# Kernel optimization log

Hardware: AMD Instinct MI355X
Metric: run time of the kernel (lower is better)

Reference implementation:

```python
import jax, jax.numpy as jnp
import numpy as np

B, S, D, H, DK, DV = 2, 2048, 1024, 16, 64, 64


def setup_inputs() -> dict:
    key = jax.random.key(0)
    ks = jax.random.split(key, 12)
    inp = {
        "query": jax.random.normal(ks[0], (B, S, D), jnp.float32),
        "key":   jax.random.normal(ks[1], (B, S, D), jnp.float32),
        "value": jax.random.normal(ks[2], (B, S, D), jnp.float32),
        # additive mask broadcast over per-head [B,S,S] scores (zeros = no masking)
        "mask":  jnp.zeros((S, S), jnp.float32),
        # stacked per-head projection params (math-equivalent to H separate Linears)
        "Wq": jax.random.normal(ks[3], (H, D, DK), jnp.float32) / np.sqrt(D),
        "bq": jax.random.normal(ks[4], (H, DK), jnp.float32) * 0.02,
        "Wk": jax.random.normal(ks[5], (H, D, DK), jnp.float32) / np.sqrt(D),
        "bk": jax.random.normal(ks[6], (H, DK), jnp.float32) * 0.02,
        "Wv": jax.random.normal(ks[7], (H, D, DV), jnp.float32) / np.sqrt(D),
        "bv": jax.random.normal(ks[8], (H, DV), jnp.float32) * 0.02,
        "Wo": jax.random.normal(ks[9], (H * DV, D), jnp.float32) / np.sqrt(H * DV),
        "bo": jax.random.normal(ks[10], (D,), jnp.float32) * 0.02,
    }
    return inp


def reference(query, key, value, mask, Wq, bq, Wk, bk, Wv, bv, Wo, bo):
    # per-head projections, vectorized over heads
    q = jnp.einsum("bsd,hdk->bhsk", query, Wq) + bq[None, :, None, :]
    k = jnp.einsum("bsd,hdk->bhsk", key, Wk) + bk[None, :, None, :]
    v = jnp.einsum("bsd,hdv->bhsv", value, Wv) + bv[None, :, None, :]
    # explicit QK^T softmax V, scale by sqrt(dim_k) (key.size(-1))
    scores = jnp.einsum("bhsk,bhtk->bhst", q, k) / jnp.sqrt(jnp.asarray(DK, q.dtype))
    scores = scores + mask  # broadcast [S,S] -> [B,H,S,S]
    attn = jax.nn.softmax(scores, axis=-1)
    out = jnp.einsum("bhst,bhtv->bhsv", attn, v)
    # concat heads along last dim: [B,S,H*DV]
    out = out.transpose(0, 2, 1, 3).reshape(B, S, H * DV)
    return out @ Wo + bo
```

## Files before the change

kernel.cpp:

```cpp
#include <hip/hip_runtime.h>
#include <stdint.h>

typedef __bf16 bf16;
typedef float f32x4 __attribute__((ext_vector_type(4)));
typedef __bf16 bf16x8 __attribute__((ext_vector_type(8)));
typedef __bf16 bf16x4 __attribute__((ext_vector_type(4)));

__device__ __forceinline__ void async_load16(const void* g, void* l) {
    __builtin_amdgcn_global_load_lds(
        (const __attribute__((address_space(1))) void*)g,
        (__attribute__((address_space(3))) void*)l, 16, 0, 0);
}

__global__ void detect_dtype(const unsigned short* __restrict__ q, int* __restrict__ flag) {
    __shared__ int cnt;
    if (threadIdx.x == 0) cnt = 0;
    __syncthreads();
    int c = 0;
    for (int i = threadIdx.x; i < 4096; i += 256) {
        int e = (q[i] >> 7) & 0xFF;
        if (e >= 0xC0) ++c;
    }
    atomicAdd(&cnt, c);
    __syncthreads();
    if (threadIdx.x == 0) { flag[0] = (cnt > 64) ? 1 : 0; flag[1] = 0; }
}

__global__ void maskscan(const unsigned int* __restrict__ m,
                         const int* __restrict__ flag, int* __restrict__ nz) {
    const int f = flag[0];
    const long nvec = (f ? 4194304L : 2097152L) / 4;
    unsigned int acc = 0;
    long stride = (long)gridDim.x * blockDim.x;
    for (long i = (long)blockIdx.x * blockDim.x + threadIdx.x; i < nvec; i += stride) {
        uint4 v = ((const uint4*)m)[i];
        acc |= v.x | v.y | v.z | v.w;
    }
    if (acc) atomicOr(nz, 1);
}

__global__ void convert2(const void* __restrict__ x0, const void* __restrict__ x1,
                         bf16* __restrict__ o0, bf16* __restrict__ o1,
                         const int* __restrict__ flag) {
    const int f = *flag;
    const void* x = blockIdx.z ? x1 : x0;
    bf16* o = blockIdx.z ? o1 : o0;
    size_t i = ((size_t)blockIdx.x * 256 + threadIdx.x) * 8;
    if (f) {
        f32x4 a = ((const f32x4*)x)[i / 4];
        f32x4 b = ((const f32x4*)x)[i / 4 + 1];
        bf16x8 v;
        for (int j = 0; j < 4; ++j) { v[j] = (bf16)a[j]; v[4 + j] = (bf16)b[j]; }
        *(bf16x8*)(o + i) = v;
    } else {
        *(bf16x8*)(o + i) = *(const bf16x8*)((const bf16*)x + i);
    }
}

__global__ void transpose_w3(const void* __restrict__ w0, const void* __restrict__ w1,
                             const void* __restrict__ w2, bf16* __restrict__ out,
                             const int* __restrict__ flag) {
    __shared__ bf16 t[32][33];
    const int f = *flag;
    const int z = blockIdx.z, src = z >> 4, sub = z & 15;
    const void* in = (src == 0) ? w0 : ((src == 1) ? w1 : w2);
    size_t base = (size_t)sub * 65536;
    int c0 = blockIdx.x * 32, r0 = blockIdx.y * 32;
    int tx = threadIdx.x, ty = threadIdx.y;
    if (f) {
        const float* inF = (const float*)in;
        for (int i = 0; i < 32; i += 8)
            t[ty + i][tx] = (bf16)inF[base + (size_t)(r0 + ty + i) * 64 + (c0 + tx)];
    } else {
        const bf16* inB = (const bf16*)in;
        for (int i = 0; i < 32; i += 8)
            t[ty + i][tx] = inB[base + (size_t)(r0 + ty + i) * 64 + (c0 + tx)];
    }
    __syncthreads();
    bf16* o = out + (size_t)z * 65536;
    for (int i = 0; i < 32; i += 8)
        o[(size_t)(c0 + ty + i) * 1024 + (r0 + tx)] = t[tx][ty + i];
}

__global__ void transpose_wo(const void* __restrict__ in, bf16* __restrict__ out,
                             const int* __restrict__ flag) {
    __shared__ bf16 t[32][33];
    const int f = *flag;
    int c0 = blockIdx.x * 32, r0 = blockIdx.y * 32;
    int tx = threadIdx.x, ty = threadIdx.y;
    if (f) {
        const float* inF = (const float*)in;
        for (int i = 0; i < 32; i += 8)
            t[ty + i][tx] = (bf16)inF[(size_t)(r0 + ty + i) * 1024 + (c0 + tx)];
    } else {
        const bf16* inB = (const bf16*)in;
        for (int i = 0; i < 32; i += 8)
            t[ty + i][tx] = inB[(size_t)(r0 + ty + i) * 1024 + (c0 + tx)];
    }
    __syncthreads();
    for (int i = 0; i < 32; i += 8)
        out[(size_t)(c0 + ty + i) * 1024 + (r0 + tx)] = t[tx][ty + i];
}

__global__ __launch_bounds__(256, 3) void gemm_qkv_b(
    const bf16* __restrict__ A0, const bf16* __restrict__ A1,
    const bf16* __restrict__ Bt,
    const void* __restrict__ b0, const void* __restrict__ b1, const void* __restrict__ b2,
    bf16* __restrict__ Qp, bf16* __restrict__ Kp, bf16* __restrict__ Vt,
    const int* __restrict__ flag, int zbase) {
    __shared__ __attribute__((aligned(16))) bf16 As[128 * 64];
    __shared__ __attribute__((aligned(16))) bf16 Bs[128 * 64];

    const int f = flag[0];
    const int K = 1024, N = 1024;
    const int z = zbase + blockIdx.z;
    const bf16* A    = blockIdx.z ? A1 : A0;
    const void* bias = (z == 0) ? b0 : ((z == 1) ? b1 : b2);
    const bf16* B    = Bt + (size_t)z * 1024 * 1024;

    const int tid  = threadIdx.x;
    const int lane = tid & 63;
    const int w    = tid >> 6;
    const int quad = lane >> 4;
    const int mrow = lane & 15;
    const int m0 = blockIdx.y * 128;
    const int n0 = blockIdx.x * 128;
    const int wm = (w & 1) * 64;
    const int wn = (w >> 1) * 64;

    f32x4 acc[4][4] = {};

    for (int k0 = 0; k0 < K; k0 += 64) {
        for (int it = 0; it < 4; ++it) {
            int ci  = it * 256 + tid;
            int row = ci >> 3, pc = ci & 7;
            int gc  = pc ^ (row & 7);
            async_load16(A + (size_t)(m0 + row) * K + k0 + gc * 8,
                         As + (size_t)(it * 256 + w * 64) * 8);
            async_load16(B + (size_t)(n0 + row) * K + k0 + gc * 8,
                         Bs + (size_t)(it * 256 + w * 64) * 8);
        }
        __syncthreads();
        for (int kk = 0; kk < 2; ++kk) {
            bf16x8 afr[4], bfr[4];
            for (int mi = 0; mi < 4; ++mi) {
                int row = wm + mi * 16 + mrow;
                int pc  = (kk * 4 + quad) ^ (row & 7);
                afr[mi] = *(const bf16x8*)(As + row * 64 + pc * 8);
            }
            for (int ni = 0; ni < 4; ++ni) {
                int row = wn + ni * 16 + mrow;
                int pc  = (kk * 4 + quad) ^ (row & 7);
                bfr[ni] = *(const bf16x8*)(Bs + row * 64 + pc * 8);
            }
            for (int mi = 0; mi < 4; ++mi)
                for (int ni = 0; ni < 4; ++ni)
                    acc[mi][ni] = __builtin_amdgcn_mfma_f32_16x16x32_bf16(
                        afr[mi], bfr[ni], acc[mi][ni], 0, 0, 0);
        }
        __syncthreads();
    }

    const float scl = (z == 0) ? 0.18033688f : 1.0f;
    for (int ni = 0; ni < 4; ++ni) {
        int n    = n0 + wn + ni * 16 + mrow;
        float bv = f ? ((const float*)bias)[n] : (float)((const bf16*)bias)[n];
        for (int mi = 0; mi < 4; ++mi) {
            int mb = m0 + wm + mi * 16 + quad * 4;
            if (z == 2) {
                bf16x4 pk;
                for (int r = 0; r < 4; ++r) pk[r] = (bf16)(acc[mi][ni][r] + bv);
                *(bf16x4*)(Vt + (((size_t)(mb >> 11) * 1024 + n) << 11) + (mb & 2047)) = pk;
            } else {
                bf16* P = (z == 0) ? Qp : Kp;
                for (int r = 0; r < 4; ++r)
                    P[(size_t)(mb + r) * N + n] = (bf16)((acc[mi][ni][r] + bv) * scl);
            }
        }
    }
}

__global__ __launch_bounds__(256, 2) void gemm_out(
    const bf16* __restrict__ A, const bf16* __restrict__ Bt,
    const void* __restrict__ bias, void* __restrict__ Cout,
    const int* __restrict__ flag) {
    __shared__ __attribute__((aligned(16))) bf16 As[128 * 64];
    __shared__ __attribute__((aligned(16))) bf16 Bs[64 * 64];

    const int f = flag[0];
    const int K = 1024, N = 1024;
    const int tid  = threadIdx.x;
    const int lane = tid & 63;
    const int w    = tid >> 6;
    const int quad = lane >> 4;
    const int mrow = lane & 15;
    const int m0 = blockIdx.y * 128;
    const int n0 = blockIdx.x * 64;
    const int wm = (w & 1) * 64;
    const int wn = (w >> 1) * 32;

    f32x4 acc[4][2] = {};

    for (int k0 = 0; k0 < K; k0 += 64) {
        for (int it = 0; it < 4; ++it) {
            int ci  = it * 256 + tid;
            int row = ci >> 3, pc = ci & 7;
            int gc  = pc ^ (row & 7);
            async_load16(A + (size_t)(m0 + row) * K + k0 + gc * 8,
                         As + (size_t)(it * 256 + w * 64) * 8);
        }
        for (int it = 0; it < 2; ++it) {
            int ci  = it * 256 + tid;
            int row = ci >> 3, pc = ci & 7;
            int gc  = pc ^ (row & 7);
            async_load16(Bt + (size_t)(n0 + row) * K + k0 + gc * 8,
                         Bs + (size_t)(it * 256 + w * 64) * 8);
        }
        __syncthreads();
        for (int kk = 0; kk < 2; ++kk) {
            bf16x8 afr[4], bfr[2];
            for (int mi = 0; mi < 4; ++mi) {
                int row = wm + mi * 16 + mrow;
                int pc  = (kk * 4 + quad) ^ (row & 7);
                afr[mi] = *(const bf16x8*)(As + row * 64 + pc * 8);
            }
            for (int ni = 0; ni < 2; ++ni) {
                int row = wn + ni * 16 + mrow;
                int pc  = (kk * 4 + quad) ^ (row & 7);
                bfr[ni] = *(const bf16x8*)(Bs + row * 64 + pc * 8);
            }
            for (int mi = 0; mi < 4; ++mi)
                for (int ni = 0; ni < 2; ++ni)
                    acc[mi][ni] = __builtin_amdgcn_mfma_f32_16x16x32_bf16(
                        afr[mi], bfr[ni], acc[mi][ni], 0, 0, 0);
        }
        __syncthreads();
    }

    for (int ni = 0; ni < 2; ++ni) {
        int n    = n0 + wn + ni * 16 + mrow;
        float bv = f ? ((const float*)bias)[n] : (float)((const bf16*)bias)[n];
        for (int mi = 0; mi < 4; ++mi) {
            int mb = m0 + wm + mi * 16 + quad * 4;
            for (int r = 0; r < 4; ++r) {
                float val = acc[mi][ni][r] + bv;
                if (f) ((float*)Cout)[(size_t)(mb + r) * N + n] = val;
                else   ((bf16*)Cout)[(size_t)(mb + r) * N + n] = (bf16)val;
            }
        }
    }
}

__global__ __launch_bounds__(256, 3) void flash_attn(
    const bf16* __restrict__ Qp, const bf16* __restrict__ Kp,
    const bf16* __restrict__ Vt, const void* __restrict__ maskv,
    bf16* __restrict__ O, const int* __restrict__ flag) {
    __shared__ __attribute__((aligned(16))) bf16 Ks[2][4096];
    __shared__ __attribute__((aligned(16))) bf16 Vs[2][4096];
    __shared__ __attribute__((aligned(16))) bf16 Ps[64 * 72];

    const int f       = flag[0];
    const int useMask = flag[1];
    const int tid  = threadIdx.x;
    const int lane = tid & 63;
    const int w    = tid >> 6;
    const int quad = lane >> 4;
    const int c    = lane & 15;
    const int s0   = blockIdx.x * 64;
    const int h    = blockIdx.y;
    const int b    = blockIdx.z;

    const size_t qkBase = (size_t)b * 2048 * 1024 + h * 64;
    const size_t vtBase = ((size_t)b * 1024 + h * 64) * 2048;

    const int ci0 = tid, ci1 = 256 + tid;
    const int r0 = ci0 >> 3, g0 = (ci0 & 7) ^ (r0 & 7);
    const int r1 = ci1 >> 3, g1 = (ci1 & 7) ^ (r1 & 7);
    const bf16* kp0 = Kp + qkBase + (size_t)r0 * 1024 + g0 * 8;
    const bf16* kp1 = Kp + qkBase + (size_t)r1 * 1024 + g1 * 8;
    const bf16* vp0 = Vt + vtBase + (size_t)r0 * 2048 + g0 * 8;
    const bf16* vp1 = Vt + vtBase + (size_t)r1 * 2048 + g1 * 8;

#define STAGE(B_, T_) do {                                              \
        async_load16(kp0 + (size_t)(T_) * 1024, &Ks[B_][(size_t)(w * 64) * 8]);        \
        async_load16(kp1 + (size_t)(T_) * 1024, &Ks[B_][(size_t)(256 + w * 64) * 8]);  \
        async_load16(vp0 + (T_),                &Vs[B_][(size_t)(w * 64) * 8]);        \
        async_load16(vp1 + (T_),                &Vs[B_][(size_t)(256 + w * 64) * 8]);  \
    } while (0)

    const bf16* kf0 = &Ks[0][c * 64 + ((0 + quad) ^ (c & 7)) * 8];
    const bf16* kf1 = &Ks[0][c * 64 + ((4 + quad) ^ (c & 7)) * 8];
    const bf16* vf0 = &Vs[0][c * 64 + ((0 + quad) ^ (c & 7)) * 8];
    const bf16* vf1 = &Vs[0][c * 64 + ((4 + quad) ^ (c & 7)) * 8];
    bf16*       pw  = Ps + (w * 16 + c) * 72 + quad * 4;
    const bf16* pr  = Ps + (w * 16 + c) * 72 + quad * 8;

    bf16x8 aq[2];
    {
        const bf16* qrow = Qp + qkBase + (size_t)(s0 + w * 16 + c) * 1024;
        aq[0] = *(const bf16x8*)(qrow + quad * 8);
        aq[1] = *(const bf16x8*)(qrow + 32 + quad * 8);
    }

    f32x4 o_acc[4] = {};
    float l_s = 0.f;

    const size_t mbase = (size_t)(s0 + w * 16 + c) * 2048;

#define FCOMP(IB_, T_) do {                                                         \
        f32x4 sc[4] = {};                                                           \
        _Pragma("unroll") for (int tt = 0; tt < 4; ++tt) {                          \
            bf16x8 ak0 = *(const bf16x8*)(kf0 + (IB_) * 4096 + tt * 1024);          \
            bf16x8 ak1 = *(const bf16x8*)(kf1 + (IB_) * 4096 + tt * 1024);          \
            sc[tt] = __builtin_amdgcn_mfma_f32_16x16x32_bf16(ak0, aq[0], sc[tt], 0, 0, 0); \
            sc[tt] = __builtin_amdgcn_mfma_f32_16x16x32_bf16(ak1, aq[1], sc[tt], 0, 0, 0); \
        }                                                                           \
        if (useMask) {                                                              \
            const size_t mr = mbase + (T_);                                         \
            _Pragma("unroll") for (int tt = 0; tt < 4; ++tt) {                      \
                if (f) {                                                            \
                    f32x4 mk = *(const f32x4*)((const float*)maskv + mr + tt * 16 + quad * 4); \
                    for (int r = 0; r < 4; ++r) sc[tt][r] += mk[r] * 1.44269504f;   \
                } else {                                                            \
                    bf16x4 mk = *(const bf16x4*)((const bf16*)maskv + mr + tt * 16 + quad * 4); \
                    for (int r = 0; r < 4; ++r) sc[tt][r] += (float)mk[r] * 1.44269504f; \
                }                                                                   \
            }                                                                       \
        }                                                                           \
        float rsum = 0.f;                                                           \
        _Pragma("unroll") for (int tt = 0; tt < 4; ++tt) {                          \
            bf16x4 pk;                                                              \
            for (int r = 0; r < 4; ++r) {                                           \
                float p = exp2f(sc[tt][r]);                                         \
                rsum += p;                                                          \
                pk[r] = (bf16)p;                                                    \
            }                                                                       \
            *(bf16x4*)(pw + tt * 16) = pk;                                          \
        }                                                                           \
        l_s += rsum;                                                                \
        _Pragma("unroll") for (int kk = 0; kk < 2; ++kk) {                          \
            bf16x8 ap = *(const bf16x8*)(pr + kk * 32);                             \
            const bf16* vfb = kk ? vf1 : vf0;                                       \
            _Pragma("unroll") for (int ni = 0; ni < 4; ++ni) {                      \
                bf16x8 bv = *(const bf16x8*)(vfb + (IB_) * 4096 + ni * 1024);       \
                o_acc[ni] = __builtin_amdgcn_mfma_f32_16x16x32_bf16(ap, bv, o_acc[ni], 0, 0, 0); \
            }                                                                       \
        }                                                                           \
    } while (0)

    STAGE(0, 0);
    for (int t0 = 0; t0 < 2048; t0 += 128) {
        __syncthreads();
        STAGE(1, t0 + 64);
        FCOMP(0, t0);
        __syncthreads();
        if (t0 + 128 < 2048) STAGE(0, t0 + 128);
        FCOMP(1, t0 + 64);
    }
#undef STAGE
#undef FCOMP

    l_s += __shfl_xor(l_s, 16, 64);
    l_s += __shfl_xor(l_s, 32, 64);
    float lrow[4];
    for (int r = 0; r < 4; ++r) lrow[r] = __shfl(l_s, quad * 4 + r, 64);
    for (int r = 0; r < 4; ++r) {
        float inv   = 1.0f / lrow[r];
        size_t roff = (size_t)(b * 2048 + s0 + w * 16 + quad * 4 + r) * 1024 + h * 64;
        for (int ni = 0; ni < 4; ++ni)
            O[roff + ni * 16 + c] = (bf16)(o_acc[ni][r] * inv);
    }
}

extern "C" void kernel_launch(void* const* d_in, const int* in_sizes, int n_in,
                              void* d_out, int out_size, void* d_ws, size_t ws_size,
                              hipStream_t stream) {
    bf16* ws = (bf16*)d_ws;
    (void)in_sizes; (void)n_in; (void)out_size; (void)ws_size;

    const size_t MM = 1024 * 1024;
    int*  flag = (int*)ws;
    bf16* WqT  = ws + 8;
    bf16* WoT  = WqT + 3 * MM;
    bf16* Qp   = WoT + MM;
    bf16* Kp   = Qp + 4 * MM;
    bf16* AO   = Kp + 4 * MM;
    bf16* Xc1  = AO;
    bf16* Vt   = (bf16*)d_out;
    bf16* Xc2  = (bf16*)d_out + 4 * MM;

    detect_dtype<<<1, 256, 0, stream>>>((const unsigned short*)d_in[0], flag);
    maskscan<<<1024, 256, 0, stream>>>((const unsigned int*)d_in[3], flag, flag + 1);

    dim3 tb(32, 8, 1);
    transpose_w3<<<dim3(2, 32, 48), tb, 0, stream>>>(d_in[4], d_in[6], d_in[8], WqT, flag);
    transpose_wo<<<dim3(32, 32, 1), tb, 0, stream>>>(d_in[10], WoT, flag);

    convert2<<<dim3(2048, 1, 2), 256, 0, stream>>>(d_in[0], d_in[1], Xc1, Xc2, flag);
    gemm_qkv_b<<<dim3(8, 32, 2), 256, 0, stream>>>(Xc1, Xc2, WqT,
                                                   d_in[5], d_in[7], d_in[9],
                                                   Qp, Kp, Vt, flag, 0);
    convert2<<<dim3(2048, 1, 1), 256, 0, stream>>>(d_in[2], d_in[2], Xc1, Xc1, flag);
    gemm_qkv_b<<<dim3(8, 32, 1), 256, 0, stream>>>(Xc1, Xc1, WqT,
                                                   d_in[5], d_in[7], d_in[9],
                                                   Qp, Kp, Vt, flag, 2);

    flash_attn<<<dim3(32, 16, 2), 256, 0, stream>>>(Qp, Kp, Vt, d_in[3], AO, flag);

    gemm_out<<<dim3(16, 32, 1), 256, 0, stream>>>(AO, WoT, d_in[11], d_out, flag);
}
```

Before: 303.3 us.

## Fuse prep kernels, single QKV GEMM launch, 128-row flash attention tiles

Merges mask scan, input conversion and all weight transposes into one multi-task prep kernel. The three QKV projections now run in one GEMM launch, with the key input read directly as fp32 and converted to bf16 in LDS instead of via a separate convert pass. Flash attention doubles the query rows per block to 128 so each K/V tile loaded into LDS is reused by twice as many MFMAs, and occupancy is lowered to 2 blocks per CU. This cuts launch count and memory traffic but raises register and LDS pressure in attention and widens the fp32 A tile in the GEMM.

```diff
diff --git a/kernel.cpp b/kernel.cpp
--- a/kernel.cpp
+++ b/kernel.cpp
@@ -26,95 +26,93 @@
     if (threadIdx.x == 0) { flag[0] = (cnt > 64) ? 1 : 0; flag[1] = 0; }
 }
 
-__global__ void maskscan(const unsigned int* __restrict__ m,
-                         const int* __restrict__ flag, int* __restrict__ nz) {
-    const int f = flag[0];
-    const long nvec = (f ? 4194304L : 2097152L) / 4;
-    unsigned int acc = 0;
-    long stride = (long)gridDim.x * blockDim.x;
-    for (long i = (long)blockIdx.x * blockDim.x + threadIdx.x; i < nvec; i += stride) {
-        uint4 v = ((const uint4*)m)[i];
-        acc |= v.x | v.y | v.z | v.w;
-    }
-    if (acc) atomicOr(nz, 1);
-}
-
-__global__ void convert2(const void* __restrict__ x0, const void* __restrict__ x1,
-                         bf16* __restrict__ o0, bf16* __restrict__ o1,
-                         const int* __restrict__ flag) {
-    const int f = *flag;
-    const void* x = blockIdx.z ? x1 : x0;
-    bf16* o = blockIdx.z ? o1 : o0;
-    size_t i = ((size_t)blockIdx.x * 256 + threadIdx.x) * 8;
-    if (f) {
-        f32x4 a = ((const f32x4*)x)[i / 4];
-        f32x4 b = ((const f32x4*)x)[i / 4 + 1];
-        bf16x8 v;
-        for (int j = 0; j < 4; ++j) { v[j] = (bf16)a[j]; v[4 + j] = (bf16)b[j]; }
-        *(bf16x8*)(o + i) = v;
+__global__ void prep(const void* __restrict__ qv, const void* __restrict__ vv,
+                     const void* __restrict__ wq, const void* __restrict__ wk,
+                     const void* __restrict__ wv, const void* __restrict__ wo,
+                     const unsigned int* __restrict__ mask,
+                     bf16* __restrict__ Xq, bf16* __restrict__ Xv,
+                     bf16* __restrict__ WqT, bf16* __restrict__ WoT,
+                     int* __restrict__ flag) {
+    __shared__ bf16 t[32][33];
+    const int f    = flag[0];
+    const int task = blockIdx.z;
+    const int bid  = blockIdx.x + 64 * blockIdx.y;
+
+    if (task < 2) {
+        const void* x = task ? vv : qv;
+        bf16* o = task ? Xv : Xq;
+        size_t i = ((size_t)bid * 256 + threadIdx.x) * 8;
+        if (f) {
+            f32x4 a = ((const f32x4*)x)[i / 4];
+            f32x4 b = ((const f32x4*)x)[i / 4 + 1];
+            bf16x8 v;
+            for (int j = 0; j < 4; ++j) { v[j] = (bf16)a[j]; v[4 + j] = (bf16)b[j]; }
+            *(bf16x8*)(o + i) = v;
+        } else {
+            *(bf16x8*)(o + i) = *(const bf16x8*)((const bf16*)x + i);
+        }
+    } else if (task < 5) {
+        if (bid >= 1024) return;
+        const void* in = (task == 2) ? wq : ((task == 3) ? wk : wv);
+        int sub = bid >> 6, rem = bid & 63;
+        int c0 = (rem & 1) * 32, r0 = (rem >> 1) * 32;
+        int tx = threadIdx.x & 31, ty = threadIdx.x >> 5;
+        size_t base = (size_t)sub * 65536;
+        if (f) {
+            const float* inF = (const float*)in;
+            for (int i = 0; i < 32; i += 8)
+                t[ty + i][tx] = (bf16)inF[base + (size_t)(r0 + ty + i) * 64 + (c0 + tx)];
+        } else {
+            const bf16* inB = (const bf16*)in;
+            for (int i = 0; i < 32; i += 8)
+                t[ty + i][tx] = inB[base + (size_t)(r0 + ty + i) * 64 + (c0 + tx)];
+        }
+        __syncthreads();
+        bf16* o = WqT + ((size_t)(task - 2) * 16 + sub) * 65536;
+        for (int i = 0; i < 32; i += 8)
+            o[(size_t)(c0 + ty + i) * 1024 + (r0 + tx)] = t[tx][ty + i];
+    } else if (task == 5) {
+        if (bid >= 1024) return;
+        int c0 = (bid & 31) * 32, r0 = (bid >> 5) * 32;
+        int tx = threadIdx.x & 31, ty = threadIdx.x >> 5;
+        if (f) {
+            const float* inF = (const float*)wo;
+            for (int i = 0; i < 32; i += 8)
+                t[ty + i][tx] = (bf16)inF[(size_t)(r0 + ty + i) * 1024 + (c0 + tx)];
+        } else {
+            const bf16* inB = (const bf16*)wo;
+            for (int i = 0; i < 32; i += 8)
+                t[ty + i][tx] = inB[(size_t)(r0 + ty + i) * 1024 + (c0 + tx)];
+        }
+        __syncthreads();
+        for (int i = 0; i < 32; i += 8)
+            WoT[(size_t)(c0 + ty + i) * 1024 + (r0 + tx)] = t[tx][ty + i];
     } else {
-        *(bf16x8*)(o + i) = *(const bf16x8*)((const bf16*)x + i);
-    }
-}
-
-__global__ void transpose_w3(const void* __restrict__ w0, const void* __restrict__ w1,
-                             const void* __restrict__ w2, bf16* __restrict__ out,
-                             const int* __restrict__ flag) {
-    __shared__ bf16 t[32][33];
-    const int f = *flag;
-    const int z = blockIdx.z, src = z >> 4, sub = z & 15;
-    const void* in = (src == 0) ? w0 : ((src == 1) ? w1 : w2);
-    size_t base = (size_t)sub * 65536;
-    int c0 = blockIdx.x * 32, r0 = blockIdx.y * 32;
-    int tx = threadIdx.x, ty = threadIdx.y;
-    if (f) {
-        const float* inF = (const float*)in;
-        for (int i = 0; i < 32; i += 8)
-            t[ty + i][tx] = (bf16)inF[base + (size_t)(r0 + ty + i) * 64 + (c0 + tx)];
-    } else {
-        const bf16* inB = (const bf16*)in;
-        for (int i = 0; i < 32; i += 8)
-            t[ty + i][tx] = inB[base + (size_t)(r0 + ty + i) * 64 + (c0 + tx)];
-    }
-    __syncthreads();
-    bf16* o = out + (size_t)z * 65536;
-    for (int i = 0; i < 32; i += 8)
-        o[(size_t)(c0 + ty + i) * 1024 + (r0 + tx)] = t[tx][ty + i];
-}
-
-__global__ void transpose_wo(const void* __restrict__ in, bf16* __restrict__ out,
-                             const int* __restrict__ flag) {
-    __shared__ bf16 t[32][33];
-    const int f = *flag;
-    int c0 = blockIdx.x * 32, r0 = blockIdx.y * 32;
-    int tx = threadIdx.x, ty = threadIdx.y;
-    if (f) {
-        const float* inF = (const float*)in;
-        for (int i = 0; i < 32; i += 8)
-            t[ty + i][tx] = (bf16)inF[(size_t)(r0 + ty + i) * 1024 + (c0 + tx)];
-    } else {
-        const bf16* inB = (const bf16*)in;
-        for (int i = 0; i < 32; i += 8)
-            t[ty + i][tx] = inB[(size_t)(r0 + ty + i) * 1024 + (c0 + tx)];
-    }
-    __syncthreads();
-    for (int i = 0; i < 32; i += 8)
-        out[(size_t)(c0 + ty + i) * 1024 + (r0 + tx)] = t[tx][ty + i];
-}
-
-__global__ __launch_bounds__(256, 3) void gemm_qkv_b(
-    const bf16* __restrict__ A0, const bf16* __restrict__ A1,
-    const bf16* __restrict__ Bt,
+        const long nvec = (f ? 4194304L : 2097152L) / 4;
+        unsigned int acc = 0;
+        long stride = 2048L * 256;
+        for (long i = (long)bid * 256 + threadIdx.x; i < nvec; i += stride) {
+            uint4 v = ((const uint4*)mask)[i];
+            acc |= v.x | v.y | v.z | v.w;
+        }
+        if (acc) atomicOr(flag + 1, 1);
+    }
+}
+
+__global__ __launch_bounds__(256, 3) void gemm_qkv(
+    const bf16* __restrict__ Xq, const void* __restrict__ keyRaw,
+    const bf16* __restrict__ Xv, const bf16* __restrict__ Bt,
     const void* __restrict__ b0, const void* __restrict__ b1, const void* __restrict__ b2,
     bf16* __restrict__ Qp, bf16* __restrict__ Kp, bf16* __restrict__ Vt,
-    const int* __restrict__ flag, int zbase) {
-    __shared__ __attribute__((aligned(16))) bf16 As[128 * 64];
+    const int* __restrict__ flag) {
+    __shared__ __attribute__((aligned(16))) unsigned char AsRaw[128 * 64 * 4];
     __shared__ __attribute__((aligned(16))) bf16 Bs[128 * 64];
 
     const int f = flag[0];
     const int K = 1024, N = 1024;
-    const int z = zbase + blockIdx.z;
-    const bf16* A    = blockIdx.z ? A1 : A0;
+    const int z = blockIdx.z;
+    const int af = (z == 1) ? f : 0;
+    const void* Av   = (z == 0) ? (const void*)Xq : ((z == 1) ? keyRaw : (const void*)Xv);
     const void* bias = (z == 0) ? b0 : ((z == 1) ? b1 : b2);
     const bf16* B    = Bt + (size_t)z * 1024 * 1024;
 
@@ -131,22 +129,54 @@
     f32x4 acc[4][4] = {};
 
     for (int k0 = 0; k0 < K; k0 += 64) {
+        if (af) {
+            for (int it = 0; it < 8; ++it) {
+                int ci  = it * 256 + tid;
+                int row = ci >> 4, pc = ci & 15;
+                int swz = ((row & 7) << 1) | ((row >> 3) & 1);
+                int gc  = pc ^ swz;
+                async_load16((const float*)Av + (size_t)(m0 + row) * K + k0 + gc * 4,
+                             AsRaw + (size_t)(it * 256 + w * 64) * 16);
+            }
+        } else {
+            for (int it = 0; it < 4; ++it) {
+                int ci  = it * 256 + tid;
+                int row = ci >> 3, pc = ci & 7;
+                int gc  = pc ^ (row & 7);
+                async_load16((const bf16*)Av + (size_t)(m0 + row) * K + k0 + gc * 8,
+                             (bf16*)AsRaw + (size_t)(it * 256 + w * 64) * 8);
+            }
+        }
         for (int it = 0; it < 4; ++it) {
             int ci  = it * 256 + tid;
             int row = ci >> 3, pc = ci & 7;
             int gc  = pc ^ (row & 7);
-            async_load16(A + (size_t)(m0 + row) * K + k0 + gc * 8,
-                         As + (size_t)(it * 256 + w * 64) * 8);
             async_load16(B + (size_t)(n0 + row) * K + k0 + gc * 8,
                          Bs + (size_t)(it * 256 + w * 64) * 8);
         }
         __syncthreads();
         for (int kk = 0; kk < 2; ++kk) {
             bf16x8 afr[4], bfr[4];
-            for (int mi = 0; mi < 4; ++mi) {
-                int row = wm + mi * 16 + mrow;
-                int pc  = (kk * 4 + quad) ^ (row & 7);
-                afr[mi] = *(const bf16x8*)(As + row * 64 + pc * 8);
+            if (af) {
+                const float* Asf = (const float*)AsRaw;
+                for (int mi = 0; mi < 4; ++mi) {
+                    int row = wm + mi * 16 + mrow;
+                    int swz = ((row & 7) << 1) | ((row >> 3) & 1);
+                    int lc  = (kk * 4 + quad) * 2;
+                    f32x4 u0 = *(const f32x4*)(Asf + row * 64 + (lc ^ swz) * 4);
+                    f32x4 u1 = *(const f32x4*)(Asf + row * 64 + ((lc + 1) ^ swz) * 4);
+                    for (int j = 0; j < 4; ++j) {
+                        afr[mi][j]     = (bf16)u0[j];
+                        afr[mi][4 + j] = (bf16)u1[j];
+                    }
+                }
+            } else {
+                const bf16* Asb = (const bf16*)AsRaw;
+                for (int mi = 0; mi < 4; ++mi) {
+                    int row = wm + mi * 16 + mrow;
+                    int pc  = (kk * 4 + quad) ^ (row & 7);
+                    afr[mi] = *(const bf16x8*)(Asb + row * 64 + pc * 8);
+                }
             }
             for (int ni = 0; ni < 4; ++ni) {
                 int row = wn + ni * 16 + mrow;
@@ -251,13 +281,13 @@
     }
 }
 
-__global__ __launch_bounds__(256, 3) void flash_attn(
+__global__ __launch_bounds__(256, 2) void flash_attn(
     const bf16* __restrict__ Qp, const bf16* __restrict__ Kp,
     const bf16* __restrict__ Vt, const void* __restrict__ maskv,
     bf16* __restrict__ O, const int* __restrict__ flag) {
     __shared__ __attribute__((aligned(16))) bf16 Ks[2][4096];
     __shared__ __attribute__((aligned(16))) bf16 Vs[2][4096];
-    __shared__ __attribute__((aligned(16))) bf16 Ps[64 * 72];
+    __shared__ __attribute__((aligned(16))) bf16 Ps[128 * 72];
 
     const int f       = flag[0];
     const int useMask = flag[1];
@@ -266,7 +296,7 @@
     const int w    = tid >> 6;
     const int quad = lane >> 4;
     const int c    = lane & 15;
-    const int s0   = blockIdx.x * 64;
+    const int s0   = blockIdx.x * 128;
     const int h    = blockIdx.y;
     const int b    = blockIdx.z;
 
@@ -281,7 +311,7 @@
     const bf16* vp0 = Vt + vtBase + (size_t)r0 * 2048 + g0 * 8;
     const bf16* vp1 = Vt + vtBase + (size_t)r1 * 2048 + g1 * 8;
 
-#define STAGE(B_, T_) do {                                              \
+#define STAGE(B_, T_) do {                                                             \
         async_load16(kp0 + (size_t)(T_) * 1024, &Ks[B_][(size_t)(w * 64) * 8]);        \
         async_load16(kp1 + (size_t)(T_) * 1024, &Ks[B_][(size_t)(256 + w * 64) * 8]);  \
         async_load16(vp0 + (T_),                &Vs[B_][(size_t)(w * 64) * 8]);        \
@@ -292,60 +322,72 @@
     const bf16* kf1 = &Ks[0][c * 64 + ((4 + quad) ^ (c & 7)) * 8];
     const bf16* vf0 = &Vs[0][c * 64 + ((0 + quad) ^ (c & 7)) * 8];
     const bf16* vf1 = &Vs[0][c * 64 + ((4 + quad) ^ (c & 7)) * 8];
-    bf16*       pw  = Ps + (w * 16 + c) * 72 + quad * 4;
-    const bf16* pr  = Ps + (w * 16 + c) * 72 + quad * 8;
-
-    bf16x8 aq[2];
-    {
-        const bf16* qrow = Qp + qkBase + (size_t)(s0 + w * 16 + c) * 1024;
-        aq[0] = *(const bf16x8*)(qrow + quad * 8);
-        aq[1] = *(const bf16x8*)(qrow + 32 + quad * 8);
-    }
-
-    f32x4 o_acc[4] = {};
-    float l_s = 0.f;
-
-    const size_t mbase = (size_t)(s0 + w * 16 + c) * 2048;
-
-#define FCOMP(IB_, T_) do {                                                         \
-        f32x4 sc[4] = {};                                                           \
-        _Pragma("unroll") for (int tt = 0; tt < 4; ++tt) {                          \
-            bf16x8 ak0 = *(const bf16x8*)(kf0 + (IB_) * 4096 + tt * 1024);          \
-            bf16x8 ak1 = *(const bf16x8*)(kf1 + (IB_) * 4096 + tt * 1024);          \
-            sc[tt] = __builtin_amdgcn_mfma_f32_16x16x32_bf16(ak0, aq[0], sc[tt], 0, 0, 0); \
-            sc[tt] = __builtin_amdgcn_mfma_f32_16x16x32_bf16(ak1, aq[1], sc[tt], 0, 0, 0); \
-        }                                                                           \
-        if (useMask) {                                                              \
-            const size_t mr = mbase + (T_);                                         \
-            _Pragma("unroll") for (int tt = 0; tt < 4; ++tt) {                      \
-                if (f) {                                                            \
-                    f32x4 mk = *(const f32x4*)((const float*)maskv + mr + tt * 16 + quad * 4); \
-                    for (int r = 0; r < 4; ++r) sc[tt][r] += mk[r] * 1.44269504f;   \
-                } else {                                                            \
-                    bf16x4 mk = *(const bf16x4*)((const bf16*)maskv + mr + tt * 16 + quad * 4); \
-                    for (int r = 0; r < 4; ++r) sc[tt][r] += (float)mk[r] * 1.44269504f; \
-                }                                                                   \
-            }                                                                       \
-        }                                                                           \
-        float rsum = 0.f;                                                           \
-        _Pragma("unroll") for (int tt = 0; tt < 4; ++tt) {                          \
-            bf16x4 pk;                                                              \
-            for (int r = 0; r < 4; ++r) {                                           \
-                float p = exp2f(sc[tt][r]);                                         \
-                rsum += p;                                                          \
-                pk[r] = (bf16)p;                                                    \
-            }                                                                       \
-            *(bf16x4*)(pw + tt * 16) = pk;                                          \
-        }                                                                           \
-        l_s += rsum;                                                                \
-        _Pragma("unroll") for (int kk = 0; kk < 2; ++kk) {                          \
-            bf16x8 ap = *(const bf16x8*)(pr + kk * 32);                             \
-            const bf16* vfb = kk ? vf1 : vf0;                                       \
-            _Pragma("unroll") for (int ni = 0; ni < 4; ++ni) {                      \
-                bf16x8 bv = *(const bf16x8*)(vfb + (IB_) * 4096 + ni * 1024);       \
-                o_acc[ni] = __builtin_amdgcn_mfma_f32_16x16x32_bf16(ap, bv, o_acc[ni], 0, 0, 0); \
-            }                                                                       \
-        }                                                                           \
+    bf16*       pw0 = Ps + (w * 32 + c) * 72 + quad * 4;
+    bf16*       pw1 = Ps + (w * 32 + 16 + c) * 72 + quad * 4;
+    const bf16* pr0 = Ps + (w * 32 + c) * 72 + quad * 8;
+    const bf16* pr1 = Ps + (w * 32 + 16 + c) * 72 + quad * 8;
+
+    bf16x8 aq[2][2];
+    for (int hh = 0; hh < 2; ++hh) {
+        const bf16* qrow = Qp + qkBase + (size_t)(s0 + w * 32 + hh * 16 + c) * 1024;
+        aq[hh][0] = *(const bf16x8*)(qrow + quad * 8);
+        aq[hh][1] = *(const bf16x8*)(qrow + 32 + quad * 8);
+    }
+
+    f32x4 o_acc[2][4] = {};
+    float l_s[2] = {0.f, 0.f};
+
+    const size_t mb0 = (size_t)(s0 + w * 32 + c) * 2048;
+    const size_t mb1 = (size_t)(s0 + w * 32 + 16 + c) * 2048;
+
+#define FCOMP(IB_, T_) do {                                                              \
+        f32x4 sc[2][4] = {};                                                             \
+        _Pragma("unroll") for (int tt = 0; tt < 4; ++tt) {                               \
+            bf16x8 ak0 = *(const bf16x8*)(kf0 + (IB_) * 4096 + tt * 1024);               \
+            bf16x8 ak1 = *(const bf16x8*)(kf1 + (IB_) * 4096 + tt * 1024);               \
+            sc[0][tt] = __builtin_amdgcn_mfma_f32_16x16x32_bf16(ak0, aq[0][0], sc[0][tt], 0, 0, 0); \
+            sc[0][tt] = __builtin_amdgcn_mfma_f32_16x16x32_bf16(ak1, aq[0][1], sc[0][tt], 0, 0, 0); \
+            sc[1][tt] = __builtin_amdgcn_mfma_f32_16x16x32_bf16(ak0, aq[1][0], sc[1][tt], 0, 0, 0); \
+            sc[1][tt] = __builtin_amdgcn_mfma_f32_16x16x32_bf16(ak1, aq[1][1], sc[1][tt], 0, 0, 0); \
+        }                                                                                \
+        if (useMask) {                                                                   \
+            _Pragma("unroll") for (int hh = 0; hh < 2; ++hh) {                           \
+                const size_t mr = (hh ? mb1 : mb0) + (T_);                               \
+                _Pragma("unroll") for (int tt = 0; tt < 4; ++tt) {                       \
+                    if (f) {                                                             \
+                        f32x4 mk = *(const f32x4*)((const float*)maskv + mr + tt * 16 + quad * 4); \
+                        for (int r = 0; r < 4; ++r) sc[hh][tt][r] += mk[r] * 1.44269504f; \
+                    } else {                                                             \
+                        bf16x4 mk = *(const bf16x4*)((const bf16*)maskv + mr + tt * 16 + quad * 4); \
+                        for (int r = 0; r < 4; ++r) sc[hh][tt][r] += (float)mk[r] * 1.44269504f; \
+                    }                                                                    \
+                }                                                                        \
+            }                                                                            \
+        }                                                                                \
+        _Pragma("unroll") for (int hh = 0; hh < 2; ++hh) {                               \
+            float rsum = 0.f;                                                            \
+            bf16* pw = hh ? pw1 : pw0;                                                   \
+            _Pragma("unroll") for (int tt = 0; tt < 4; ++tt) {                           \
+                bf16x4 pk;                                                               \
+                for (int r = 0; r < 4; ++r) {                                            \
+                    float p = exp2f(sc[hh][tt][r]);                                      \
+                    rsum += p;                                                           \
+                    pk[r] = (bf16)p;                                                     \
+                }                                                                        \
+                *(bf16x4*)(pw + tt * 16) = pk;                                           \
+            }                                                                            \
+            l_s[hh] += rsum;                                                             \
+        }                                                                                \
+        _Pragma("unroll") for (int kk = 0; kk < 2; ++kk) {                               \
+            bf16x8 ap0 = *(const bf16x8*)((kk ? pr0 + 32 : pr0));                        \
+            bf16x8 ap1 = *(const bf16x8*)((kk ? pr1 + 32 : pr1));                        \
+            const bf16* vfb = kk ? vf1 : vf0;                                            \
+            _Pragma("unroll") for (int ni = 0; ni < 4; ++ni) {                           \
+                bf16x8 bv = *(const bf16x8*)(vfb + (IB_) * 4096 + ni * 1024);            \
+                o_acc[0][ni] = __builtin_amdgcn_mfma_f32_16x16x32_bf16(ap0, bv, o_acc[0][ni], 0, 0, 0); \
+                o_acc[1][ni] = __builtin_amdgcn_mfma_f32_16x16x32_bf16(ap1, bv, o_acc[1][ni], 0, 0, 0); \
+            }                                                                            \
+        }                                                                                \
     } while (0)
 
     STAGE(0, 0);
@@ -360,15 +402,17 @@
 #undef STAGE
 #undef FCOMP
 
-    l_s += __shfl_xor(l_s, 16, 64);
-    l_s += __shfl_xor(l_s, 32, 64);
-    float lrow[4];
-    for (int r = 0; r < 4; ++r) lrow[r] = __shfl(l_s, quad * 4 + r, 64);
-    for (int r = 0; r < 4; ++r) {
-        float inv   = 1.0f / lrow[r];
-        size_t roff = (size_t)(b * 2048 + s0 + w * 16 + quad * 4 + r) * 1024 + h * 64;
-        for (int ni = 0; ni < 4; ++ni)
-            O[roff + ni * 16 + c] = (bf16)(o_acc[ni][r] * inv);
+    for (int hh = 0; hh < 2; ++hh) {
+        float ls = l_s[hh];
+        ls += __shfl_xor(ls, 16, 64);
+        ls += __shfl_xor(ls, 32, 64);
+        for (int r = 0; r < 4; ++r) {
+            float lv   = __shfl(ls, quad * 4 + r, 64);
+            float inv  = 1.0f / lv;
+            size_t roff = (size_t)(b * 2048 + s0 + w * 32 + hh * 16 + quad * 4 + r) * 1024 + h * 64;
+            for (int ni = 0; ni < 4; ++ni)
+                O[roff + ni * 16 + c] = (bf16)(o_acc[hh][ni][r] * inv);
+        }
     }
 }
 
@@ -384,28 +428,23 @@
     bf16* WoT  = WqT + 3 * MM;
     bf16* Qp   = WoT + MM;
     bf16* Kp   = Qp + 4 * MM;
-    bf16* AO   = Kp + 4 * MM;
-    bf16* Xc1  = AO;
-    bf16* Vt   = (bf16*)d_out;
-    bf16* Xc2  = (bf16*)d_out + 4 * MM;
+    bf16* Xq   = Kp + 4 * MM;
+    bf16* AO   = Xq;
+    bf16* Xv   = (bf16*)d_out;
+    bf16* Vt   = (bf16*)d_out + 4 * MM;
 
     detect_dtype<<<1, 256, 0, stream>>>((const unsigned short*)d_in[0], flag);
-    maskscan<<<1024, 256, 0, stream>>>((const unsigned int*)d_in[3], flag, flag + 1);
-
-    dim3 tb(32, 8, 1);
-    transpose_w3<<<dim3(2, 32, 48), tb, 0, stream>>>(d_in[4], d_in[6], d_in[8], WqT, flag);
-    transpose_wo<<<dim3(32, 32, 1), tb, 0, stream>>>(d_in[10], WoT, flag);
-
-    convert2<<<dim3(2048, 1, 2), 256, 0, stream>>>(d_in[0], d_in[1], Xc1, Xc2, flag);
-    gemm_qkv_b<<<dim3(8, 32, 2), 256, 0, stream>>>(Xc1, Xc2, WqT,
-                                                   d_in[5], d_in[7], d_in[9],
-                                                   Qp, Kp, Vt, flag, 0);
-    convert2<<<dim3(2048, 1, 1), 256, 0, stream>>>(d_in[2], d_in[2], Xc1, Xc1, flag);
-    gemm_qkv_b<<<dim3(8, 32, 1), 256, 0, stream>>>(Xc1, Xc1, WqT,
-                                                   d_in[5], d_in[7], d_in[9],
-                                                   Qp, Kp, Vt, flag, 2);
-
-    flash_attn<<<dim3(32, 16, 2), 256, 0, stream>>>(Qp, Kp, Vt, d_in[3], AO, flag);
+
+    prep<<<dim3(64, 32, 7), 256, 0, stream>>>(d_in[0], d_in[2], d_in[4], d_in[6],
+                                              d_in[8], d_in[10],
+                                              (const unsigned int*)d_in[3],
+                                              Xq, Xv, WqT, WoT, flag);
+
+    gemm_qkv<<<dim3(8, 32, 3), 256, 0, stream>>>(Xq, d_in[1], Xv, WqT,
+                                                 d_in[5], d_in[7], d_in[9],
+                                                 Qp, Kp, Vt, flag);
+
+    flash_attn<<<dim3(16, 16, 2), 256, 0, stream>>>(Qp, Kp, Vt, d_in[3], AO, flag);
 
     gemm_out<<<dim3(16, 32, 1), 256, 0, stream>>>(AO, WoT, d_in[11], d_out, flag);
 }
```

After: 268.8 us. 11.4% less time.
